# Optimization experiments

Hardware: AMD Instinct MI355X
Metric: run time of the kernel (lower is better)

The kernel has to match this reference:

```python
import jax, jax.numpy as jnp
import numpy as np
from jax import lax

B, C_IN, H, W = 16, 64, 128, 128
KH, KW, C_OUT = 3, 3, 128


def setup_inputs() -> dict:
    key = jax.random.key(0)
    k1, k2, k3, k4, k5 = jax.random.split(key, 5)
    x = jax.random.normal(k1, (B, C_IN, H, W), jnp.float32)
    # xavier-uniform-ish weight, layout [kh*kw*C_in, C_out] with patch ordering (kh, kw, c)
    limit = np.sqrt(6.0 / (KH * KW * C_IN + C_OUT)).astype(np.float32)
    w = jax.random.uniform(k2, (KH * KW * C_IN, C_OUT), jnp.float32, -limit, limit)
    b = jax.random.uniform(k3, (C_OUT,), jnp.float32)
    q = jax.random.uniform(k4, (1,), jnp.float32)
    p = jax.random.uniform(k5, (1,), jnp.float32)
    return {"x": x, "w": w, "b": b, "q": q, "p": p}


def reference(x, w, b, q, p):
    # Fused implicit-GEMM form of SCS: patch dot products and patch norms are
    # both expressed as convolutions, avoiding the im2col blowup.
    qe = jnp.exp(q[0])
    pe = jnp.exp(p[0])
    # torch patch layout after unfold+moveaxis is (kh, kw, C); w rows follow it
    w_conv = w.reshape(KH, KW, C_IN, C_OUT)  # HWIO
    dn = lax.conv_dimension_numbers(x.shape, w_conv.shape, ('NCHW', 'HWIO', 'NCHW'))
    pad = [(1, 1), (1, 1)]  # pad_len = k-1 = 2, split lo//2, rest (same as torch code)
    # s . k  -> [B, C_out, H, W]
    s_dot_k = lax.conv_general_dilated(x, w_conv, (1, 1), pad, dimension_numbers=dn)
    # ||s||_2 per patch (over kh, kw, C) -> [B, 1, H, W]
    ones_k = jnp.ones((KH, KW, C_IN, 1), x.dtype)
    patch_sq = lax.conv_general_dilated(x * x, ones_k, (1, 1), pad, dimension_numbers=dn)
    norm_s_q = jnp.sqrt(patch_sq) + qe
    norm_k_q = jnp.linalg.norm(w) + qe  # Frobenius norm of the whole weight matrix
    sim = s_dot_k / (norm_s_q * norm_k_q)
    out = jnp.sign(s_dot_k) * jnp.abs(sim) ** pe + b[None, :, None, None]
    return out  # [B, C_out, H, W]
```

## Files before the change

kernel.cpp:

```cpp
#include <hip/hip_runtime.h>
#include <hip/hip_bf16.h>
#include <math.h>

#define B_N 16
#define C_IN 64
#define H_N 128
#define W_N 128
#define C_OUT 128

typedef __attribute__((ext_vector_type(8))) short short8v;
typedef __attribute__((ext_vector_type(4))) float float4v;

__device__ __forceinline__ unsigned short f2bf(float f) {
  union { float f; unsigned u; } c; c.f = f;
  unsigned u = c.u + 0x7fffu + ((c.u >> 16) & 1u);
  return (unsigned short)(u >> 16);
}

__global__ __launch_bounds__(256) void scs_prep_w(
    const float* __restrict__ w, unsigned short* __restrict__ wf,
    float* __restrict__ partial)
{
  __shared__ float red[256];
  const int t    = threadIdx.x;
  const int gid  = blockIdx.x * 256 + t;
  const int frag = gid >> 6;
  const int l    = gid & 63;
  const int kh   = frag / 48;
  const int rem  = frag % 48;
  const int s    = rem >> 3;
  const int nt   = rem & 7;
  const int kb   = kh * 192 + s * 32 + (l >> 4) * 8;
  const int n    = nt * 16 + (l & 15);
  short8v pk;
  float ss = 0.f;
#pragma unroll
  for (int j = 0; j < 8; ++j) {
    const float v = w[(size_t)(kb + j) * C_OUT + n];
    ss = fmaf(v, v, ss);
    pk[j] = (short)f2bf(v);
  }
  *reinterpret_cast<short8v*>(wf + (size_t)frag * 512 + l * 8) = pk;
  red[t] = ss;
  __syncthreads();
  for (int off = 128; off > 0; off >>= 1) {
    if (t < off) red[t] += red[t + off];
    __syncthreads();
  }
  if (t == 0) partial[blockIdx.x] = red[0];
}

__global__ __launch_bounds__(512, 4) void scs_main(
    const float* __restrict__ x, const unsigned short* __restrict__ wf,
    const float* __restrict__ bias, const float* __restrict__ q,
    const float* __restrict__ p, const float* __restrict__ partial,
    float* __restrict__ out)
{
  __shared__ alignas(16) char xT[4 * 16640];
  __shared__ float psacc[4][4][128];
  __shared__ float pl[2][128];

  const int t   = threadIdx.x;
  const int l   = t & 63;
  const int wid = t >> 6;
  const int wm  = wid >> 2;
  const int wn  = wid & 3;
  const int lr  = l & 15;
  const int lg  = l >> 4;
  const int bid = blockIdx.x;
  const int swz = (bid & 7) * 128 + (bid >> 3);
  const int b   = swz >> 6;
  const int h0  = (swz & 63) << 1;

  if (t < 64) {
    const int k   = t >> 3;
    const int row = k >> 1;
    const int jr  = (k & 1) ? 129 : 0;
    *reinterpret_cast<float4v*>(xT + row * 16640 + jr * 128 + (t & 7) * 16) =
        float4v{0.f, 0.f, 0.f, 0.f};
  }

  const int wcol  = t & 127;
  const int cbase = t >> 7;
  float part0 = 0.f, part1 = 0.f, part2 = 0.f, part3 = 0.f;
#pragma unroll
  for (int it = 0; it < 8; ++it) {
    const int  row4  = it >> 1;
    const int  cc    = (it & 1) * 4 + cbase;
    const int  inr   = h0 - 1 + row4;
    const bool valid = (unsigned)inr < 128u;
    const int  jr    = wcol + 1;
    int byte = row4 * 16640 + jr * 128 + cc * 16;
    byte ^= (jr & 7) << 4;
    if (valid) {
      const float* src = x + (((size_t)b * C_IN + cc * 8) * H_N + inr) * W_N + wcol;
      float xv[8];
#pragma unroll
      for (int j = 0; j < 8; ++j)
        xv[j] = src[(size_t)j * H_N * W_N];
      float pp = 0.f;
#pragma unroll
      for (int j = 0; j < 8; ++j) pp = fmaf(xv[j], xv[j], pp);
      if      (row4 == 0) part0 += pp;
      else if (row4 == 1) part1 += pp;
      else if (row4 == 2) part2 += pp;
      else                part3 += pp;
      union { __hip_bfloat162 h2[4]; short8v v; } pk;
#pragma unroll
      for (int j = 0; j < 4; ++j)
        pk.h2[j] = __float22bfloat162_rn(make_float2(xv[2 * j], xv[2 * j + 1]));
      *reinterpret_cast<short8v*>(xT + byte) = pk.v;
    } else {
      *reinterpret_cast<short8v*>(xT + byte) = short8v{0,0,0,0,0,0,0,0};
    }
  }
  psacc[cbase][0][wcol] = part0;
  psacc[cbase][1][wcol] = part1;
  psacc[cbase][2][wcol] = part2;
  psacc[cbase][3][wcol] = part3;

  const float bv0 = bias[wn * 32 + lr];
  const float bv1 = bias[wn * 32 + 16 + lr];

  __syncthreads();

  float4v acc[2][4][2];
#pragma unroll
  for (int o = 0; o < 2; ++o)
#pragma unroll
    for (int ml = 0; ml < 4; ++ml)
#pragma unroll
      for (int nl = 0; nl < 2; ++nl) acc[o][ml][nl] = float4v{0.f, 0.f, 0.f, 0.f};

  const int jbase = wm * 64 + lr;
#pragma unroll
  for (int s = 0; s < 6; ++s) {
    const int kw    = s >> 1;
    const int half  = s & 1;
    const int cslot = half * 4 + lg;
    const int jlow  = (lr + kw) & 7;
    const int base_s = (jbase + kw) * 128 + ((cslot * 16) ^ (jlow << 4));

    short8v bfr[3][2];
#pragma unroll
    for (int r = 0; r < 3; ++r) {
      const int fi = (r * 6 + s) * 8 + wn * 2;
      bfr[r][0] = *reinterpret_cast<const short8v*>(wf + (size_t)(fi + 0) * 512 + l * 8);
      bfr[r][1] = *reinterpret_cast<const short8v*>(wf + (size_t)(fi + 1) * 512 + l * 8);
    }
#pragma unroll
    for (int r = 0; r < 4; ++r) {
      short8v a[4];
#pragma unroll
      for (int ml = 0; ml < 4; ++ml)
        a[ml] = *reinterpret_cast<const short8v*>(xT + base_s + r * 16640 + ml * 2048);
      if (r < 3) {
#pragma unroll
        for (int ml = 0; ml < 4; ++ml)
#pragma unroll
          for (int nl = 0; nl < 2; ++nl)
            acc[0][ml][nl] = __builtin_amdgcn_mfma_f32_16x16x32_bf16(
                a[ml], bfr[r][nl], acc[0][ml][nl], 0, 0, 0);
      }
      if (r >= 1) {
#pragma unroll
        for (int ml = 0; ml < 4; ++ml)
#pragma unroll
          for (int nl = 0; nl < 2; ++nl)
            acc[1][ml][nl] = __builtin_amdgcn_mfma_f32_16x16x32_bf16(
                a[ml], bfr[r - 1][nl], acc[1][ml][nl], 0, 0, 0);
      }
    }
  }

  float ssum = 0.f;
#pragma unroll
  for (int i = 0; i < 36; ++i) ssum += partial[i];
  const float nk = sqrtf(ssum);
  const float qe = __builtin_amdgcn_exp2f(q[0] * 1.4426950408889634f);
  const float pe = __builtin_amdgcn_exp2f(p[0] * 1.4426950408889634f);
  const float nlg_nkq = -__builtin_amdgcn_logf(nk + qe);

  if (t < 256) {
    const int o = t >> 7;
    const int w = t & 127;
    float P = 0.f;
#pragma unroll
    for (int dw = 0; dw < 3; ++dw) {
      const int ww = w + dw - 1;
      if ((unsigned)ww < 128u) {
#pragma unroll
        for (int rr = 0; rr < 3; ++rr)
#pragma unroll
          for (int cc = 0; cc < 4; ++cc)
            P += psacc[cc][o + rr][ww];
      }
    }
    pl[o][w] = pe * (nlg_nkq - __builtin_amdgcn_logf(sqrtf(P) + qe));
  }
  __syncthreads();

#pragma unroll
  for (int o = 0; o < 2; ++o) {
    const int oh = h0 + o;
#pragma unroll
    for (int ml = 0; ml < 4; ++ml) {
      const int w0 = wm * 64 + ml * 16 + lg * 4;
      const float4v plv = *reinterpret_cast<const float4v*>(&pl[o][w0]);
#pragma unroll
      for (int nl = 0; nl < 2; ++nl) {
        const int n  = wn * 32 + nl * 16 + lr;
        const float bv = nl ? bv1 : bv0;
        float4v ov;
#pragma unroll
        for (int r = 0; r < 4; ++r) {
          const float sv  = acc[o][ml][nl][r];
          const float lg2 = __builtin_amdgcn_logf(fabsf(sv));
          const float e   = __builtin_amdgcn_exp2f(fmaf(pe, lg2, plv[r]));
          ov[r] = copysignf(e, sv) + bv;
        }
        *reinterpret_cast<float4v*>(
            out + (((size_t)b * C_OUT + n) * H_N + oh) * W_N + w0) = ov;
      }
    }
  }
}

extern "C" void kernel_launch(void* const* d_in, const int* in_sizes, int n_in,
                              void* d_out, int out_size, void* d_ws, size_t ws_size,
                              hipStream_t stream) {
  const float* x = (const float*)d_in[0];
  const float* w = (const float*)d_in[1];
  const float* b = (const float*)d_in[2];
  const float* q = (const float*)d_in[3];
  const float* p = (const float*)d_in[4];
  float* out = (float*)d_out;
  float* partial = (float*)d_ws;
  unsigned short* wf = (unsigned short*)((char*)d_ws + 256);

  scs_prep_w<<<36, 256, 0, stream>>>(w, wf, partial);
  scs_main<<<B_N * (H_N / 2), 512, 0, stream>>>(x, wf, b, q, p, partial, out);
}
```

Measured before the change: 59.63 us.

## Split output tile along width into 64-column halves to double block count

Each block now covers 2 output rows by 64 columns instead of 2 by 128, so there are twice as many blocks, each using about half the shared memory. Launch bounds move to 6 blocks per CU to raise occupancy. Halo columns are loaded separately, including zero padding at the image edge, and the patch-norm reduction is reworked over 8 channel groups. In exchange, each block loads relatively more halo data and each wave does half the MFMA work per weight fragment load, so weight reuse drops.

After: 65.63 us. 10.1% more time.

```diff
diff --git a/kernel.cpp b/kernel.cpp
--- a/kernel.cpp
+++ b/kernel.cpp
@@ -50,15 +50,17 @@
   if (t == 0) partial[blockIdx.x] = red[0];
 }
 
-__global__ __launch_bounds__(512, 4) void scs_main(
+#define RS 8448
+
+__global__ __launch_bounds__(512, 6) void scs_main(
     const float* __restrict__ x, const unsigned short* __restrict__ wf,
     const float* __restrict__ bias, const float* __restrict__ q,
     const float* __restrict__ p, const float* __restrict__ partial,
     float* __restrict__ out)
 {
-  __shared__ alignas(16) char xT[4 * 16640];
-  __shared__ float psacc[4][4][128];
-  __shared__ float pl[2][128];
+  __shared__ alignas(16) char xT[4 * RS];
+  __shared__ float psacc[8][4][66];
+  __shared__ float pl[2][64];
 
   const int t   = threadIdx.x;
   const int l   = t & 63;
@@ -68,71 +70,84 @@
   const int lr  = l & 15;
   const int lg  = l >> 4;
   const int bid = blockIdx.x;
-  const int swz = (bid & 7) * 128 + (bid >> 3);
-  const int b   = swz >> 6;
-  const int h0  = (swz & 63) << 1;
-
+  const int swz = (bid & 7) * 256 + (bid >> 3);
+  const int b   = swz >> 7;
+  const int h0  = ((swz >> 1) & 63) << 1;
+  const int w0  = (swz & 1) << 6;
+
+  const int wl = t & 63;
+  const int g  = t >> 3 & 0;
+  const int gg = t >> 6;
+  {
+    const int jr  = wl + 1;
+    int xbyte0 = jr * 128 + gg * 16;
+    xbyte0 ^= (jr & 7) << 4;
+#pragma unroll
+    for (int r = 0; r < 4; ++r) {
+      const int  inr   = h0 - 1 + r;
+      const bool valid = (unsigned)inr < 128u;
+      float ss = 0.f;
+      if (valid) {
+        const float* src = x + (((size_t)b * C_IN + gg * 8) * H_N + inr) * W_N + w0 + wl;
+        float xv[8];
+#pragma unroll
+        for (int j = 0; j < 8; ++j) xv[j] = src[(size_t)j * H_N * W_N];
+#pragma unroll
+        for (int j = 0; j < 8; ++j) ss = fmaf(xv[j], xv[j], ss);
+        union { __hip_bfloat162 h2[4]; short8v v; } pk;
+#pragma unroll
+        for (int j = 0; j < 4; ++j)
+          pk.h2[j] = __float22bfloat162_rn(make_float2(xv[2 * j], xv[2 * j + 1]));
+        *reinterpret_cast<short8v*>(xT + r * RS + xbyte0) = pk.v;
+      } else {
+        *reinterpret_cast<short8v*>(xT + r * RS + xbyte0) = short8v{0,0,0,0,0,0,0,0};
+      }
+      psacc[gg][r][jr] = ss;
+    }
+  }
   if (t < 64) {
-    const int k   = t >> 3;
-    const int row = k >> 1;
-    const int jr  = (k & 1) ? 129 : 0;
-    *reinterpret_cast<float4v*>(xT + row * 16640 + jr * 128 + (t & 7) * 16) =
-        float4v{0.f, 0.f, 0.f, 0.f};
-  }
-
-  const int wcol  = t & 127;
-  const int cbase = t >> 7;
-  float part0 = 0.f, part1 = 0.f, part2 = 0.f, part3 = 0.f;
-#pragma unroll
-  for (int it = 0; it < 8; ++it) {
-    const int  row4  = it >> 1;
-    const int  cc    = (it & 1) * 4 + cbase;
-    const int  inr   = h0 - 1 + row4;
-    const bool valid = (unsigned)inr < 128u;
-    const int  jr    = wcol + 1;
-    int byte = row4 * 16640 + jr * 128 + cc * 16;
-    byte ^= (jr & 7) << 4;
+    const int e  = t & 1;
+    const int r  = (t >> 1) & 3;
+    const int g2 = t >> 3;
+    const int jr = e ? 65 : 0;
+    const int gw = w0 - 1 + e * 65;
+    const int inr = h0 - 1 + r;
+    const bool valid = ((unsigned)inr < 128u) && ((unsigned)gw < 128u);
+    float ss = 0.f;
+    int xbyte = r * RS + jr * 128 + g2 * 16;
+    xbyte ^= (jr & 7) << 4;
     if (valid) {
-      const float* src = x + (((size_t)b * C_IN + cc * 8) * H_N + inr) * W_N + wcol;
+      const float* src = x + (((size_t)b * C_IN + g2 * 8) * H_N + inr) * W_N + gw;
       float xv[8];
 #pragma unroll
-      for (int j = 0; j < 8; ++j)
-        xv[j] = src[(size_t)j * H_N * W_N];
-      float pp = 0.f;
-#pragma unroll
-      for (int j = 0; j < 8; ++j) pp = fmaf(xv[j], xv[j], pp);
-      if      (row4 == 0) part0 += pp;
-      else if (row4 == 1) part1 += pp;
-      else if (row4 == 2) part2 += pp;
-      else                part3 += pp;
+      for (int j = 0; j < 8; ++j) xv[j] = src[(size_t)j * H_N * W_N];
+#pragma unroll
+      for (int j = 0; j < 8; ++j) ss = fmaf(xv[j], xv[j], ss);
       union { __hip_bfloat162 h2[4]; short8v v; } pk;
 #pragma unroll
       for (int j = 0; j < 4; ++j)
         pk.h2[j] = __float22bfloat162_rn(make_float2(xv[2 * j], xv[2 * j + 1]));
-      *reinterpret_cast<short8v*>(xT + byte) = pk.v;
+      *reinterpret_cast<short8v*>(xT + xbyte) = pk.v;
     } else {
-      *reinterpret_cast<short8v*>(xT + byte) = short8v{0,0,0,0,0,0,0,0};
-    }
-  }
-  psacc[cbase][0][wcol] = part0;
-  psacc[cbase][1][wcol] = part1;
-  psacc[cbase][2][wcol] = part2;
-  psacc[cbase][3][wcol] = part3;
+      *reinterpret_cast<short8v*>(xT + xbyte) = short8v{0,0,0,0,0,0,0,0};
+    }
+    psacc[g2][r][jr] = ss;
+  }
 
   const float bv0 = bias[wn * 32 + lr];
   const float bv1 = bias[wn * 32 + 16 + lr];
 
   __syncthreads();
 
-  float4v acc[2][4][2];
+  float4v acc[2][2][2];
 #pragma unroll
   for (int o = 0; o < 2; ++o)
 #pragma unroll
-    for (int ml = 0; ml < 4; ++ml)
+    for (int ml = 0; ml < 2; ++ml)
 #pragma unroll
       for (int nl = 0; nl < 2; ++nl) acc[o][ml][nl] = float4v{0.f, 0.f, 0.f, 0.f};
 
-  const int jbase = wm * 64 + lr;
+  const int jbase = wm * 32 + lr;
 #pragma unroll
   for (int s = 0; s < 6; ++s) {
     const int kw    = s >> 1;
@@ -150,13 +165,13 @@
     }
 #pragma unroll
     for (int r = 0; r < 4; ++r) {
-      short8v a[4];
-#pragma unroll
-      for (int ml = 0; ml < 4; ++ml)
-        a[ml] = *reinterpret_cast<const short8v*>(xT + base_s + r * 16640 + ml * 2048);
+      short8v a[2];
+#pragma unroll
+      for (int ml = 0; ml < 2; ++ml)
+        a[ml] = *reinterpret_cast<const short8v*>(xT + base_s + r * RS + ml * 2048);
       if (r < 3) {
 #pragma unroll
-        for (int ml = 0; ml < 4; ++ml)
+        for (int ml = 0; ml < 2; ++ml)
 #pragma unroll
           for (int nl = 0; nl < 2; ++nl)
             acc[0][ml][nl] = __builtin_amdgcn_mfma_f32_16x16x32_bf16(
@@ -164,7 +179,7 @@
       }
       if (r >= 1) {
 #pragma unroll
-        for (int ml = 0; ml < 4; ++ml)
+        for (int ml = 0; ml < 2; ++ml)
 #pragma unroll
           for (int nl = 0; nl < 2; ++nl)
             acc[1][ml][nl] = __builtin_amdgcn_mfma_f32_16x16x32_bf16(
@@ -181,21 +196,15 @@
   const float pe = __builtin_amdgcn_exp2f(p[0] * 1.4426950408889634f);
   const float nlg_nkq = -__builtin_amdgcn_logf(nk + qe);
 
-  if (t < 256) {
-    const int o = t >> 7;
-    const int w = t & 127;
+  if (t < 128) {
+    const int o = t >> 6;
+    const int w = t & 63;
     float P = 0.f;
 #pragma unroll
-    for (int dw = 0; dw < 3; ++dw) {
-      const int ww = w + dw - 1;
-      if ((unsigned)ww < 128u) {
-#pragma unroll
-        for (int rr = 0; rr < 3; ++rr)
-#pragma unroll
-          for (int cc = 0; cc < 4; ++cc)
-            P += psacc[cc][o + rr][ww];
-      }
-    }
+    for (int rr = 0; rr < 3; ++rr)
+#pragma unroll
+      for (int cc = 0; cc < 8; ++cc)
+        P += psacc[cc][o + rr][w] + psacc[cc][o + rr][w + 1] + psacc[cc][o + rr][w + 2];
     pl[o][w] = pe * (nlg_nkq - __builtin_amdgcn_logf(sqrtf(P) + qe));
   }
   __syncthreads();
@@ -204,9 +213,9 @@
   for (int o = 0; o < 2; ++o) {
     const int oh = h0 + o;
 #pragma unroll
-    for (int ml = 0; ml < 4; ++ml) {
-      const int w0 = wm * 64 + ml * 16 + lg * 4;
-      const float4v plv = *reinterpret_cast<const float4v*>(&pl[o][w0]);
+    for (int ml = 0; ml < 2; ++ml) {
+      const int wloc = wm * 32 + ml * 16 + lg * 4;
+      const float4v plv = *reinterpret_cast<const float4v*>(&pl[o][wloc]);
 #pragma unroll
       for (int nl = 0; nl < 2; ++nl) {
         const int n  = wn * 32 + nl * 16 + lr;
@@ -220,7 +229,7 @@
           ov[r] = copysignf(e, sv) + bv;
         }
         *reinterpret_cast<float4v*>(
-            out + (((size_t)b * C_OUT + n) * H_N + oh) * W_N + w0) = ov;
+            out + (((size_t)b * C_OUT + n) * H_N + oh) * W_N + w0 + wloc) = ov;
       }
     }
   }
@@ -239,5 +248,5 @@
   unsigned short* wf = (unsigned short*)((char*)d_ws + 256);
 
   scs_prep_w<<<36, 256, 0, stream>>>(w, wf, partial);
-  scs_main<<<B_N * (H_N / 2), 512, 0, stream>>>(x, wf, b, q, p, partial, out);
-}
+  scs_main<<<B_N * H_N, 512, 0, stream>>>(x, wf, b, q, p, partial, out);
+}
```

## Pre-transpose input to bf16 global buffer and run GEMM reading A from global

Applied to the files above, without the earlier changes.

Adds a prep kernel that converts x to a padded, channel-slotted bf16 layout in workspace and precomputes 3-wide row sums of squared values. The main kernel then reads A fragments straight from global memory (no LDS staging), using smaller tiles (64-wide output columns, 2048 blocks) and a cheap 3-row sum for patch norms. This removes the per-block transposition and the redundant 4-row halo reloads, but adds an extra global round trip of the converted input (about 35MB written and read) and an extra launch. The old kernel is kept as a fallback when the workspace is too small.

After: 89.41 us. 1.5x slower.

```diff
diff --git a/kernel.cpp b/kernel.cpp
--- a/kernel.cpp
+++ b/kernel.cpp
@@ -10,12 +10,18 @@
 
 typedef __attribute__((ext_vector_type(8))) short short8v;
 typedef __attribute__((ext_vector_type(4))) float float4v;
+typedef __attribute__((ext_vector_type(4))) unsigned int uint4v;
 
 __device__ __forceinline__ unsigned short f2bf(float f) {
   union { float f; unsigned u; } c; c.f = f;
   unsigned u = c.u + 0x7fffu + ((c.u >> 16) & 1u);
   return (unsigned short)(u >> 16);
 }
+
+#define WS_WF_OFF    256
+#define WS_XTG_OFF   151552
+#define WS_SROWC_OFF (151552 + 34611200)
+#define WS_NEED      (WS_SROWC_OFF + 1064960)
 
 __global__ __launch_bounds__(256) void scs_prep_w(
     const float* __restrict__ w, unsigned short* __restrict__ wf,
@@ -50,7 +56,177 @@
   if (t == 0) partial[blockIdx.x] = red[0];
 }
 
-__global__ __launch_bounds__(512, 4) void scs_main(
+__global__ __launch_bounds__(256) void scs_prep_x(
+    const float* __restrict__ x, unsigned short* __restrict__ xTg,
+    float* __restrict__ SrowC)
+{
+  __shared__ float ps[2][128];
+  __shared__ float Srow[128];
+
+  const int t    = threadIdx.x;
+  const int bidx = blockIdx.x;
+  const int b    = bidx / 130;
+  const int hrow = bidx % 130;
+  const int h    = hrow - 1;
+  unsigned short* rowp = xTg + (size_t)(b * 130 + hrow) * 8320;
+  float* srp = SrowC + (size_t)(b * 130 + hrow) * 128;
+
+  if (h < 0 || h >= H_N) {
+    for (int i = t; i < 1040; i += 256)
+      *reinterpret_cast<short8v*>(rowp + i * 8) = short8v{0,0,0,0,0,0,0,0};
+    if (t < 128) srp[t] = 0.f;
+    return;
+  }
+
+  const int w = t & 127, chalf = t >> 7;
+  float v[32];
+  const float* src = x + (((size_t)b * C_IN + chalf * 32) * H_N + h) * W_N + w;
+#pragma unroll
+  for (int j = 0; j < 32; ++j) v[j] = src[(size_t)j * H_N * W_N];
+  float ss = 0.f;
+#pragma unroll
+  for (int j = 0; j < 32; ++j) ss = fmaf(v[j], v[j], ss);
+  ps[chalf][w] = ss;
+
+#pragma unroll
+  for (int c4 = 0; c4 < 4; ++c4) {
+    const int cslot = chalf * 4 + c4;
+    union { __hip_bfloat162 h2[4]; short8v v8; } pk;
+#pragma unroll
+    for (int k = 0; k < 4; ++k)
+      pk.h2[k] = __float22bfloat162_rn(make_float2(v[c4 * 8 + 2 * k], v[c4 * 8 + 2 * k + 1]));
+    *reinterpret_cast<short8v*>(rowp + ((size_t)cslot * 130 + w + 1) * 8) = pk.v8;
+  }
+  if (t < 16) {
+    const int cslot = t >> 1;
+    const int wsl   = (t & 1) ? 129 : 0;
+    *reinterpret_cast<short8v*>(rowp + ((size_t)cslot * 130 + wsl) * 8) =
+        short8v{0,0,0,0,0,0,0,0};
+  }
+  __syncthreads();
+  if (t < 128) Srow[t] = ps[0][t] + ps[1][t];
+  __syncthreads();
+  if (t < 128) {
+    const float lft = (t > 0)   ? Srow[t - 1] : 0.f;
+    const float rgt = (t < 127) ? Srow[t + 1] : 0.f;
+    srp[t] = lft + Srow[t] + rgt;
+  }
+}
+
+__global__ __launch_bounds__(512, 4) void scs_mainM(
+    const unsigned short* __restrict__ xTg, const unsigned short* __restrict__ wf,
+    const float* __restrict__ SrowC, const float* __restrict__ bias,
+    const float* __restrict__ q, const float* __restrict__ p,
+    const float* __restrict__ partial, float* __restrict__ out)
+{
+  __shared__ float pl[2][64];
+
+  const int t   = threadIdx.x;
+  const int l   = t & 63;
+  const int wid = t >> 6;
+  const int wm  = wid >> 2;
+  const int wn  = wid & 3;
+  const int lr  = l & 15;
+  const int lg  = l >> 4;
+  const int bid = blockIdx.x;
+  const int swz = (bid & 7) * 256 + (bid >> 3);
+  const int b   = swz >> 7;
+  const int hp  = (swz & 127) >> 1;
+  const int w0  = (swz & 1) << 6;
+  const int h0  = hp << 1;
+
+  float ssum = 0.f;
+#pragma unroll
+  for (int i = 0; i < 36; ++i) ssum += partial[i];
+  const float nk = sqrtf(ssum);
+  const float qe = __builtin_amdgcn_exp2f(q[0] * 1.4426950408889634f);
+  const float pe = __builtin_amdgcn_exp2f(p[0] * 1.4426950408889634f);
+  const float nlg_nkq = -__builtin_amdgcn_logf(nk + qe);
+  const float bv0 = bias[wn * 32 + lr];
+  const float bv1 = bias[wn * 32 + 16 + lr];
+
+  if (t < 128) {
+    const int o = t >> 6, wl = t & 63;
+    const float* sp = SrowC + ((size_t)(b * 130 + h0 + o) * 128) + w0 + wl;
+    const float P = sp[0] + sp[128] + sp[256];
+    pl[o][wl] = pe * (nlg_nkq - __builtin_amdgcn_logf(sqrtf(P) + qe));
+  }
+  __syncthreads();
+
+  float4v acc[2][2][2];
+#pragma unroll
+  for (int o = 0; o < 2; ++o)
+#pragma unroll
+    for (int ml = 0; ml < 2; ++ml)
+#pragma unroll
+      for (int nl = 0; nl < 2; ++nl) acc[o][ml][nl] = float4v{0.f, 0.f, 0.f, 0.f};
+
+  const unsigned short* abase = xTg + (size_t)(b * 130 + h0) * 8320;
+  const int jbase = w0 + wm * 32 + lr;
+#pragma unroll
+  for (int s = 0; s < 6; ++s) {
+    const int kw    = s >> 1;
+    const int cslot = (s & 1) * 4 + lg;
+    const int off_s = (cslot * 130 + jbase + kw) * 8;
+    short8v bfr[3][2];
+#pragma unroll
+    for (int r = 0; r < 3; ++r) {
+      const int fi = (r * 6 + s) * 8 + wn * 2;
+      bfr[r][0] = *reinterpret_cast<const short8v*>(wf + (size_t)(fi + 0) * 512 + l * 8);
+      bfr[r][1] = *reinterpret_cast<const short8v*>(wf + (size_t)(fi + 1) * 512 + l * 8);
+    }
+#pragma unroll
+    for (int r = 0; r < 4; ++r) {
+      short8v a[2];
+#pragma unroll
+      for (int ml = 0; ml < 2; ++ml)
+        a[ml] = *reinterpret_cast<const short8v*>(abase + (size_t)r * 8320 + off_s + ml * 128);
+      if (r < 3) {
+#pragma unroll
+        for (int ml = 0; ml < 2; ++ml)
+#pragma unroll
+          for (int nl = 0; nl < 2; ++nl)
+            acc[0][ml][nl] = __builtin_amdgcn_mfma_f32_16x16x32_bf16(
+                a[ml], bfr[r][nl], acc[0][ml][nl], 0, 0, 0);
+      }
+      if (r >= 1) {
+#pragma unroll
+        for (int ml = 0; ml < 2; ++ml)
+#pragma unroll
+          for (int nl = 0; nl < 2; ++nl)
+            acc[1][ml][nl] = __builtin_amdgcn_mfma_f32_16x16x32_bf16(
+                a[ml], bfr[r - 1][nl], acc[1][ml][nl], 0, 0, 0);
+      }
+    }
+  }
+
+#pragma unroll
+  for (int o = 0; o < 2; ++o) {
+    const int oh = h0 + o;
+#pragma unroll
+    for (int ml = 0; ml < 2; ++ml) {
+      const int wloc = wm * 32 + ml * 16 + lg * 4;
+      const float4v plv = *reinterpret_cast<const float4v*>(&pl[o][wloc]);
+#pragma unroll
+      for (int nl = 0; nl < 2; ++nl) {
+        const int n  = wn * 32 + nl * 16 + lr;
+        const float bv = nl ? bv1 : bv0;
+        float4v ov;
+#pragma unroll
+        for (int r = 0; r < 4; ++r) {
+          const float sv  = acc[o][ml][nl][r];
+          const float lg2 = __builtin_amdgcn_logf(fabsf(sv));
+          const float e   = __builtin_amdgcn_exp2f(fmaf(pe, lg2, plv[r]));
+          ov[r] = copysignf(e, sv) + bv;
+        }
+        *reinterpret_cast<float4v*>(
+            out + (((size_t)b * C_OUT + n) * H_N + oh) * W_N + w0 + wloc) = ov;
+      }
+    }
+  }
+}
+
+__global__ __launch_bounds__(512, 4) void scs_main_fb(
     const float* __restrict__ x, const unsigned short* __restrict__ wf,
     const float* __restrict__ bias, const float* __restrict__ q,
     const float* __restrict__ p, const float* __restrict__ partial,
@@ -96,8 +272,7 @@
       const float* src = x + (((size_t)b * C_IN + cc * 8) * H_N + inr) * W_N + wcol;
       float xv[8];
 #pragma unroll
-      for (int j = 0; j < 8; ++j)
-        xv[j] = src[(size_t)j * H_N * W_N];
+      for (int j = 0; j < 8; ++j) xv[j] = src[(size_t)j * H_N * W_N];
       float pp = 0.f;
 #pragma unroll
       for (int j = 0; j < 8; ++j) pp = fmaf(xv[j], xv[j], pp);
@@ -121,7 +296,6 @@
 
   const float bv0 = bias[wn * 32 + lr];
   const float bv1 = bias[wn * 32 + 16 + lr];
-
   __syncthreads();
 
   float4v acc[2][4][2];
@@ -140,7 +314,6 @@
     const int cslot = half * 4 + lg;
     const int jlow  = (lr + kw) & 7;
     const int base_s = (jbase + kw) * 128 + ((cslot * 16) ^ (jlow << 4));
-
     short8v bfr[3][2];
 #pragma unroll
     for (int r = 0; r < 3; ++r) {
@@ -236,8 +409,16 @@
   const float* p = (const float*)d_in[4];
   float* out = (float*)d_out;
   float* partial = (float*)d_ws;
-  unsigned short* wf = (unsigned short*)((char*)d_ws + 256);
+  unsigned short* wf = (unsigned short*)((char*)d_ws + WS_WF_OFF);
 
   scs_prep_w<<<36, 256, 0, stream>>>(w, wf, partial);
-  scs_main<<<B_N * (H_N / 2), 512, 0, stream>>>(x, wf, b, q, p, partial, out);
-}
+
+  if (ws_size >= (size_t)WS_NEED) {
+    unsigned short* xTg = (unsigned short*)((char*)d_ws + WS_XTG_OFF);
+    float* SrowC = (float*)((char*)d_ws + WS_SROWC_OFF);
+    scs_prep_x<<<16 * 130, 256, 0, stream>>>(x, xTg, SrowC);
+    scs_mainM<<<2048, 512, 0, stream>>>(xTg, wf, SrowC, b, q, p, partial, out);
+  } else {
+    scs_main_fb<<<B_N * (H_N / 2), 512, 0, stream>>>(x, wf, b, q, p, partial, out);
+  }
+}
```
